# Kernel optimization log

Hardware: AMD Instinct MI355X
Metric: run time of the kernel (lower is better)

Reference implementation:

```python
import jax, jax.numpy as jnp
import numpy as np

B, T, D = 4, 4096, 64

def setup_inputs() -> dict:
    key = jax.random.key(0)
    kq, kk, kv = jax.random.split(key, 3)
    Q = jax.random.normal(kq, (B, T, D), dtype=jnp.float32)
    K = jax.random.normal(kk, (B, T, D), dtype=jnp.float32)
    V = jax.random.normal(kv, (B, T, D), dtype=jnp.float32)
    mask = jnp.zeros((B, T, T), dtype=jnp.float32)
    return {"Q": Q, "K": K, "V": V, "mask": mask}

def reference(Q, K, V, mask):
    dk = Q.shape[-1]
    # NOTE: original scales by 1/dk (not 1/sqrt(dk)) -- reproduce faithfully.
    scores = jnp.einsum('btd,bsd->bts', Q, K) * (1.0 / dk)  # [B,T,T]
    scores = scores + mask
    attn = jax.nn.softmax(scores, axis=-1)
    return jnp.einsum('bts,bsd->btd', attn, V)  # [B,T,D]
```

## Files before the change

kernel.cpp:

```cpp
#include <hip/hip_runtime.h>
#include <stdint.h>

#define BB 4
#define TT 4096
#define DD 64
#define KBLK 64

typedef short short8 __attribute__((ext_vector_type(8)));
typedef float f32x4 __attribute__((ext_vector_type(4)));
typedef uint32_t u32x4 __attribute__((ext_vector_type(4)));

__device__ __forceinline__ uint16_t f2bf(float x) {
  uint32_t u = __float_as_uint(x);
  u += 0x7FFFu + ((u >> 16) & 1u);
  return (uint16_t)(u >> 16);
}
__device__ __forceinline__ float bf2f(uint16_t h) {
  return __uint_as_float(((uint32_t)h) << 16);
}
__device__ __forceinline__ uint32_t pkbf(float a, float b) {
  return (uint32_t)f2bf(a) | ((uint32_t)f2bf(b) << 16);
}

#define MFMA(a, b, c) __builtin_amdgcn_mfma_f32_16x16x32_bf16((a), (b), (c), 0, 0, 0)

__global__ __launch_bounds__(256) void prep_kernel(
    const float* __restrict__ Q, const float* __restrict__ K, const float* __restrict__ V,
    uint16_t* __restrict__ Qh, uint16_t* __restrict__ Ql,
    uint16_t* __restrict__ Kh, uint16_t* __restrict__ Kl,
    uint16_t* __restrict__ Vh, uint16_t* __restrict__ Vl) {
  __shared__ float vt[64][65];
  const int blk = blockIdx.x;
  const int b = blk >> 6;
  const int r0 = (blk & 63) << 6;
  const int t = threadIdx.x;
  const size_t base = ((size_t)b * TT + r0) * DD;
  for (int i = t; i < 64 * 64; i += 256) {
    float q = Q[base + i] * 0.015625f;
    uint16_t h = f2bf(q);
    Qh[base + i] = h;
    Ql[base + i] = f2bf(q - bf2f(h));
    float k = K[base + i];
    h = f2bf(k);
    Kh[base + i] = h;
    Kl[base + i] = f2bf(k - bf2f(h));
    int r = i >> 6, c = i & 63;
    vt[r][c] = V[base + i];
  }
  __syncthreads();
  for (int i = t; i < 64 * 64; i += 256) {
    int d = i >> 6, c = i & 63;
    float v = vt[c][d];
    uint16_t h = f2bf(v);
    size_t o = ((size_t)b * DD + d) * TT + r0 + c;
    Vh[o] = h;
    Vl[o] = f2bf(v - bf2f(h));
  }
}


#define STAGE(KH, KL, VH, VL, S0)                                              \
  do {                                                                         \
    _Pragma("unroll") for (int c = t; c < 512; c += NW * 64) {                 \
      const int cb8 = (c & ~63) * 8;           \
      const int row = c >> 3;                                                  \
      const int ssl = (c & 7) ^ (row & 7);                                     \
      const size_t ksrc = kvb + (size_t)((S0) + row) * DD + ssl * 8;           \
      const size_t vsrc = vtb + (size_t)row * TT + (S0) + ssl * 8;             \
      __builtin_amdgcn_global_load_lds(Kh + ksrc, &KH[cb8], 16, 0, 0);         \
      __builtin_amdgcn_global_load_lds(Kl + ksrc, &KL[cb8], 16, 0, 0);         \
      __builtin_amdgcn_global_load_lds(Vh + vsrc, &VH[cb8], 16, 0, 0);         \
      __builtin_amdgcn_global_load_lds(Vl + vsrc, &VL[cb8], 16, 0, 0);         \
    }                                                                          \
  } while (0)

#define LOADMASK(MK, TILE)                                                     \
  do {                                                                         \
    _Pragma("unroll") for (int q_ = 0; q_ < 4; ++q_)                           \
        MK[q_] = __builtin_nontemporal_load(                                   \
            (const f32x4*)(mprow + (size_t)(TILE) * KBLK + q_ * 16));          \
  } while (0)

#define LOADMASK_Z(MK)                                                         \
  do {                                                                         \
    _Pragma("unroll") for (int q_ = 0; q_ < 4; ++q_)                           \
        MK[q_] = (f32x4){0.f, 0.f, 0.f, 0.f};                                  \
  } while (0)

#define PACK(TT_, HA, HB, LA, LB)                                              \
  {                                                                            \
    const float a0 = s_[TT_][0], a1 = s_[TT_][1];                              \
    const float a2 = s_[TT_][2], a3 = s_[TT_][3];                              \
    const uint16_t h0 = f2bf(a0), h1 = f2bf(a1);                               \
    const uint16_t h2 = f2bf(a2), h3 = f2bf(a3);                               \
    HA = (uint32_t)h0 | ((uint32_t)h1 << 16);                                  \
    HB = (uint32_t)h2 | ((uint32_t)h3 << 16);                                  \
    LA = pkbf(a0 - bf2f(h0), a1 - bf2f(h1));                                   \
    LB = pkbf(a2 - bf2f(h2), a3 - bf2f(h3));                                   \
  }

#define XCHG(W, SA0, SB0, SA1, SB1)                                            \
  {                                                                            \
    const uint32_t A0 = __shfl(SA0, src0), A1 = __shfl(SB0, src0);             \
    const uint32_t B0 = __shfl(SA1, src0), B1 = __shfl(SB1, src0);             \
    const uint32_t A2 = __shfl(SA0, src1), A3 = __shfl(SB0, src1);             \
    const uint32_t B2 = __shfl(SA1, src1), B3 = __shfl(SB1, src1);             \
    W = (u32x4){hi2 ? B0 : A0, hi2 ? B1 : A1, hi2 ? B2 : A2, hi2 ? B3 : A3};   \
  }

#define COMPUTE(KH, KL, VH, VL, MK)                                            \
  do {                                                                         \
    f32x4 s_[4];                                                               \
    _Pragma("unroll") for (int tt = 0; tt < 4; ++tt) {                         \
      f32x4 acc = (f32x4){0.f, 0.f, 0.f, 0.f};                                 \
      const short8 bh0 = *(const short8*)&KH[(tt * 16 + lr) * 64 + sw0 * 8];   \
      const short8 bl0 = *(const short8*)&KL[(tt * 16 + lr) * 64 + sw0 * 8];   \
      acc = MFMA(bh0, qh[0], acc);                                             \
      acc = MFMA(bl0, qh[0], acc);                                             \
      acc = MFMA(bh0, ql[0], acc);                                             \
      const short8 bh1 = *(const short8*)&KH[(tt * 16 + lr) * 64 + sw1 * 8];   \
      const short8 bl1 = *(const short8*)&KL[(tt * 16 + lr) * 64 + sw1 * 8];   \
      acc = MFMA(bh1, qh[1], acc);                                             \
      acc = MFMA(bl1, qh[1], acc);                                             \
      acc = MFMA(bh1, ql[1], acc);                                             \
      s_[tt] = acc + MK[tt];                                                   \
    }                                                                          \
    float cm = fmaxf(fmaxf(fmaxf(s_[0][0], s_[0][1]), fmaxf(s_[0][2], s_[0][3])), \
                     fmaxf(fmaxf(s_[1][0], s_[1][1]), fmaxf(s_[1][2], s_[1][3]))); \
    cm = fmaxf(cm, fmaxf(fmaxf(fmaxf(s_[2][0], s_[2][1]), fmaxf(s_[2][2], s_[2][3])), \
                         fmaxf(fmaxf(s_[3][0], s_[3][1]), fmaxf(s_[3][2], s_[3][3])))); \
    cm = fmaxf(cm, __shfl_xor(cm, 16));                                        \
    cm = fmaxf(cm, __shfl_xor(cm, 32));                                        \
    if (!__all(cm <= mrow + 8.0f)) {                      \
      const float mn = fmaxf(mrow, cm);                                        \
      const float scl = __expf(mrow - mn);                                     \
      mrow = mn;                                                               \
      lrow *= scl;                                                             \
      float sj0 = __shfl(scl, lq * 4 + 0), sj1 = __shfl(scl, lq * 4 + 1);      \
      float sj2 = __shfl(scl, lq * 4 + 2), sj3 = __shfl(scl, lq * 4 + 3);      \
      _Pragma("unroll") for (int dt = 0; dt < 4; ++dt) {                       \
        o[dt][0] *= sj0; o[dt][1] *= sj1; o[dt][2] *= sj2; o[dt][3] *= sj3;    \
      }                                                                        \
    }                                                                          \
    _Pragma("unroll") for (int tt = 0; tt < 4; ++tt)                           \
        _Pragma("unroll") for (int j = 0; j < 4; ++j)                          \
            s_[tt][j] = __expf(s_[tt][j] - mrow);                              \
    float rs = ((s_[0][0] + s_[0][1]) + (s_[0][2] + s_[0][3])) +               \
               ((s_[1][0] + s_[1][1]) + (s_[1][2] + s_[1][3])) +               \
               ((s_[2][0] + s_[2][1]) + (s_[2][2] + s_[2][3])) +               \
               ((s_[3][0] + s_[3][1]) + (s_[3][2] + s_[3][3]));                \
    rs += __shfl_xor(rs, 16);                                                  \
    rs += __shfl_xor(rs, 32);                                                  \
    lrow += rs;                                                                \
    uint32_t H0a, H0b, L0a, L0b, H1a, H1b, L1a, L1b;                           \
    uint32_t H2a, H2b, L2a, L2b, H3a, H3b, L3a, L3b;                           \
    PACK(0, H0a, H0b, L0a, L0b)                                                \
    PACK(1, H1a, H1b, L1a, L1b)                                                \
    PACK(2, H2a, H2b, L2a, L2b)                                                \
    PACK(3, H3a, H3b, L3a, L3b)                                                \
    u32x4 wh0, wl0, wh1, wl1;                                                  \
    XCHG(wh0, H0a, H0b, H1a, H1b)                                              \
    XCHG(wl0, L0a, L0b, L1a, L1b)                                              \
    XCHG(wh1, H2a, H2b, H3a, H3b)                                              \
    XCHG(wl1, L2a, L2b, L3a, L3b)                                              \
    const short8 ph0 = __builtin_bit_cast(short8, wh0);                        \
    const short8 pl0 = __builtin_bit_cast(short8, wl0);                        \
    const short8 ph1 = __builtin_bit_cast(short8, wh1);                        \
    const short8 pl1 = __builtin_bit_cast(short8, wl1);                        \
    _Pragma("unroll") for (int dt = 0; dt < 4; ++dt) {                         \
      const short8 vh = *(const short8*)&VH[(dt * 16 + lr) * 64 + sw0 * 8];    \
      const short8 vl = *(const short8*)&VL[(dt * 16 + lr) * 64 + sw0 * 8];    \
      o[dt] = MFMA(ph0, vh, o[dt]);                                            \
      o[dt] = MFMA(pl0, vh, o[dt]);                                            \
      o[dt] = MFMA(ph0, vl, o[dt]);                                            \
    }                                                                          \
    _Pragma("unroll") for (int dt = 0; dt < 4; ++dt) {                         \
      const short8 vh = *(const short8*)&VH[(dt * 16 + lr) * 64 + sw1 * 8];    \
      const short8 vl = *(const short8*)&VL[(dt * 16 + lr) * 64 + sw1 * 8];    \
      o[dt] = MFMA(ph1, vh, o[dt]);                                            \
      o[dt] = MFMA(pl1, vh, o[dt]);                                            \
      o[dt] = MFMA(ph1, vl, o[dt]);                                            \
    }                                                                          \
  } while (0)

template <int NSEG, int NW>
__global__ __launch_bounds__(NW * 64, 4) void attn_kernel(
    const float* __restrict__ mask, float* __restrict__ out,
    float* __restrict__ Op, float* __restrict__ Mp, float* __restrict__ Lp,
    const uint16_t* __restrict__ Qh, const uint16_t* __restrict__ Ql,
    const uint16_t* __restrict__ Kh, const uint16_t* __restrict__ Kl,
    const uint16_t* __restrict__ Vh, const uint16_t* __restrict__ Vl) {
  constexpr int RPB = NW * 16;
  constexpr int PBH = (TT / RPB) / 2;
  constexpr int SEGLEN = TT / NSEG;
  constexpr int NIT = SEGLEN / KBLK;
  static_assert((NIT & 1) == 0, "NIT must be even for 2x-unrolled dbuf");

  __shared__ uint16_t KhA[4096], KlA[4096], VhA[4096], VlA[4096];
  __shared__ uint16_t KhB[4096], KlB[4096], VhB[4096], VlB[4096];

  const int bid = blockIdx.x;
  const int xcd = bid & 7;
  const int b = xcd >> 1;
  const int u = bid >> 3;
  const int rbl = (u % PBH) * 2 + (xcd & 1);
  const int seg = u / PBH;
  const int q0 = rbl * RPB;
  const int t = threadIdx.x;
  const int w = t >> 6;
  const int l = t & 63;
  const int lr = l & 15;
  const int lq = l >> 4;
  const int qrow = q0 + w * 16;
  const int sb = seg * SEGLEN;

  const int sw0 = lq ^ (lr & 7);
  const int sw1 = sw0 ^ 4;
  const int src0 = lr + (((2 * lq) & 3) << 4);
  const int src1 = lr + (((2 * lq + 1) & 3) << 4);
  const int hi2 = lq >> 1;

  const uint16_t* qhp = Qh + ((size_t)b * TT + qrow + lr) * DD + lq * 8;
  const uint16_t* qlp = Ql + ((size_t)b * TT + qrow + lr) * DD + lq * 8;
  short8 qh[2], ql[2];
  qh[0] = *(const short8*)(qhp);
  qh[1] = *(const short8*)(qhp + 32);
  ql[0] = *(const short8*)(qlp);
  ql[1] = *(const short8*)(qlp + 32);

  f32x4 o[4];
  float mrow = -1e30f, lrow = 0.f;
#pragma unroll
  for (int dt = 0; dt < 4; ++dt) o[dt] = (f32x4){0.f, 0.f, 0.f, 0.f};

  const float* mprow = mask + ((size_t)b * TT + qrow + lr) * TT + sb + lq * 4;
  const size_t kvb = (size_t)b * TT * DD;
  const size_t vtb = (size_t)b * DD * TT;

  f32x4 mk0[4], mk1[4];
  STAGE(KhA, KlA, VhA, VlA, sb);
  LOADMASK(mk0, 0);
  __syncthreads();

  for (int itp = 0; itp < NIT / 2; ++itp) {
    const int it0 = 2 * itp;
    STAGE(KhB, KlB, VhB, VlB, sb + (it0 + 1) * KBLK);
    LOADMASK(mk1, it0 + 1);
    COMPUTE(KhA, KlA, VhA, VlA, mk0);
    __syncthreads();
    if (it0 + 2 < NIT) {
      STAGE(KhA, KlA, VhA, VlA, sb + (it0 + 2) * KBLK);
      LOADMASK(mk0, it0 + 2);
    } else {
      LOADMASK_Z(mk0);
    }
    COMPUTE(KhB, KlB, VhB, VlB, mk1);
    __syncthreads();
  }

  if constexpr (NSEG == 1) {
    const float linv = 1.0f / lrow;
#pragma unroll
    for (int j = 0; j < 4; ++j) {
      const float inv = __shfl(linv, lq * 4 + j);
      const size_t ob = ((size_t)b * TT + qrow + lq * 4 + j) * DD + lr;
#pragma unroll
      for (int dt = 0; dt < 4; ++dt) out[ob + dt * 16] = o[dt][j] * inv;
    }
  } else {
    const int grow = b * TT + qrow;
#pragma unroll
    for (int j = 0; j < 4; ++j) {
      const size_t r = (size_t)seg * (BB * TT) + grow + lq * 4 + j;
#pragma unroll
      for (int dt = 0; dt < 4; ++dt) Op[r * 64 + dt * 16 + lr] = o[dt][j];
    }
    if (lq == 0) {
      const size_t r = (size_t)seg * (BB * TT) + grow + lr;
      Mp[r] = mrow;
      Lp[r] = lrow;
    }
  }
}

__global__ __launch_bounds__(256) void combine_kernel(
    const float* __restrict__ Op, const float* __restrict__ Mp,
    const float* __restrict__ Lp, float* __restrict__ out, int nseg) {
  const int gid = blockIdx.x * 256 + threadIdx.x;
  const int r = gid >> 6, d = gid & 63;
  constexpr int ROWS = BB * TT;
  float m = -3.0e38f;
  for (int s = 0; s < nseg; ++s) m = fmaxf(m, Mp[s * ROWS + r]);
  float num = 0.f, den = 0.f;
  for (int s = 0; s < nseg; ++s) {
    const float e = __expf(Mp[s * ROWS + r] - m);
    den += Lp[s * ROWS + r] * e;
    num += Op[((size_t)s * ROWS + r) * 64 + d] * e;
  }
  out[(size_t)r * 64 + d] = num / den;
}

extern "C" void kernel_launch(void* const* d_in, const int* in_sizes, int n_in,
                              void* d_out, int out_size, void* d_ws, size_t ws_size,
                              hipStream_t stream) {
  const float* Q = (const float*)d_in[0];
  const float* K = (const float*)d_in[1];
  const float* V = (const float*)d_in[2];
  const float* mask = (const float*)d_in[3];
  float* out = (float*)d_out;

  const size_t NE = (size_t)BB * TT * DD;
  const size_t ROWS = (size_t)BB * TT;
  uint16_t* ws = (uint16_t*)d_ws;
  uint16_t* Qh = ws;
  uint16_t* Ql = ws + NE;
  uint16_t* Kh = ws + 2 * NE;
  uint16_t* Kl = ws + 3 * NE;
  uint16_t* Vh = ws + 4 * NE;
  uint16_t* Vl = ws + 5 * NE;

  const size_t bf_bytes = 6 * NE * 2;
  const size_t per_seg = ROWS * 64 * 4 + ROWS * 2 * 4;
  int nseg = (ws_size >= bf_bytes + 4 * per_seg) ? 4
           : (ws_size >= bf_bytes + 2 * per_seg) ? 2 : 1;

  char* pbase = (char*)d_ws + bf_bytes;
  float* Op = (float*)pbase;
  float* Mp = (float*)(pbase + (size_t)nseg * ROWS * 64 * 4);
  float* Lp = Mp + (size_t)nseg * ROWS;

  prep_kernel<<<dim3(256), dim3(256), 0, stream>>>(Q, K, V, Qh, Ql, Kh, Kl, Vh, Vl);

  if (nseg == 4) {
    attn_kernel<4, 8><<<dim3(512), dim3(512), 0, stream>>>(
        mask, out, Op, Mp, Lp, Qh, Ql, Kh, Kl, Vh, Vl);
  } else if (nseg == 2) {
    attn_kernel<2, 8><<<dim3(256), dim3(512), 0, stream>>>(
        mask, out, Op, Mp, Lp, Qh, Ql, Kh, Kl, Vh, Vl);
  } else {
    attn_kernel<1, 4><<<dim3(256), dim3(256), 0, stream>>>(
        mask, out, Op, Mp, Lp, Qh, Ql, Kh, Kl, Vh, Vl);
  }
  if (nseg > 1) {
    combine_kernel<<<dim3((ROWS * 64) / 256), dim3(256), 0, stream>>>(Op, Mp, Lp, out, nseg);
  }
}
```

Measured before the change: 404.6 us.

## Process two 16-row query tiles per wave to reuse K/V LDS fragments

Each wave now handles 32 query rows as two independent 16-row tiles, so every K and V fragment read from LDS feeds MFMAs for both tiles. Workgroups shrink from 8 to 4 waves with the same total rows per block, and the launch-bounds occupancy hint drops from 4 to 2. Mask loads for the next tile are moved inside the softmax step to overlap with compute. The aim is to halve LDS read traffic per MFMA and add independent MFMA chains, at the cost of more registers and lower occupancy.

```diff
diff --git a/kernel.cpp b/kernel.cpp
--- a/kernel.cpp
+++ b/kernel.cpp
@@ -74,23 +74,17 @@
     }                                                                          \
   } while (0)
 
-#define LOADMASK(MK, TILE)                                                     \
+#define LOADMASK(MK, MPR, TILE)                                                \
   do {                                                                         \
     _Pragma("unroll") for (int q_ = 0; q_ < 4; ++q_)                           \
         MK[q_] = __builtin_nontemporal_load(                                   \
-            (const f32x4*)(mprow + (size_t)(TILE) * KBLK + q_ * 16));          \
+            (const f32x4*)((MPR) + (size_t)(TILE) * KBLK + q_ * 16));          \
   } while (0)
 
-#define LOADMASK_Z(MK)                                                         \
-  do {                                                                         \
-    _Pragma("unroll") for (int q_ = 0; q_ < 4; ++q_)                           \
-        MK[q_] = (f32x4){0.f, 0.f, 0.f, 0.f};                                  \
-  } while (0)
-
-#define PACK(TT_, HA, HB, LA, LB)                                              \
+#define PACK(S, TT_, HA, HB, LA, LB)                                           \
   {                                                                            \
-    const float a0 = s_[TT_][0], a1 = s_[TT_][1];                              \
-    const float a2 = s_[TT_][2], a3 = s_[TT_][3];                              \
+    const float a0 = S[TT_][0], a1 = S[TT_][1];                                \
+    const float a2 = S[TT_][2], a3 = S[TT_][3];                                \
     const uint16_t h0 = f2bf(a0), h1 = f2bf(a1);                               \
     const uint16_t h2 = f2bf(a2), h3 = f2bf(a3);                               \
     HA = (uint32_t)h0 | ((uint32_t)h1 << 16);                                  \
@@ -108,89 +102,104 @@
     W = (u32x4){hi2 ? B0 : A0, hi2 ? B1 : A1, hi2 ? B2 : A2, hi2 ? B3 : A3};   \
   }
 
-#define COMPUTE(KH, KL, VH, VL, MK)                                            \
+#define SMPACK(S, MK, MPR, MROW, LROW, O, PH, PL, TNEXT)                       \
   do {                                                                         \
-    f32x4 s_[4];                                                               \
-    _Pragma("unroll") for (int tt = 0; tt < 4; ++tt) {                         \
-      f32x4 acc = (f32x4){0.f, 0.f, 0.f, 0.f};                                 \
-      const short8 bh0 = *(const short8*)&KH[(tt * 16 + lr) * 64 + sw0 * 8];   \
-      const short8 bl0 = *(const short8*)&KL[(tt * 16 + lr) * 64 + sw0 * 8];   \
-      acc = MFMA(bh0, qh[0], acc);                                             \
-      acc = MFMA(bl0, qh[0], acc);                                             \
-      acc = MFMA(bh0, ql[0], acc);                                             \
-      const short8 bh1 = *(const short8*)&KH[(tt * 16 + lr) * 64 + sw1 * 8];   \
-      const short8 bl1 = *(const short8*)&KL[(tt * 16 + lr) * 64 + sw1 * 8];   \
-      acc = MFMA(bh1, qh[1], acc);                                             \
-      acc = MFMA(bl1, qh[1], acc);                                             \
-      acc = MFMA(bh1, ql[1], acc);                                             \
-      s_[tt] = acc + MK[tt];                                                   \
-    }                                                                          \
-    float cm = fmaxf(fmaxf(fmaxf(s_[0][0], s_[0][1]), fmaxf(s_[0][2], s_[0][3])), \
-                     fmaxf(fmaxf(s_[1][0], s_[1][1]), fmaxf(s_[1][2], s_[1][3]))); \
-    cm = fmaxf(cm, fmaxf(fmaxf(fmaxf(s_[2][0], s_[2][1]), fmaxf(s_[2][2], s_[2][3])), \
-                         fmaxf(fmaxf(s_[3][0], s_[3][1]), fmaxf(s_[3][2], s_[3][3])))); \
+    float cm = fmaxf(fmaxf(fmaxf(S[0][0], S[0][1]), fmaxf(S[0][2], S[0][3])),  \
+                     fmaxf(fmaxf(S[1][0], S[1][1]), fmaxf(S[1][2], S[1][3]))); \
+    cm = fmaxf(cm, fmaxf(fmaxf(fmaxf(S[2][0], S[2][1]), fmaxf(S[2][2], S[2][3])), \
+                         fmaxf(fmaxf(S[3][0], S[3][1]), fmaxf(S[3][2], S[3][3])))); \
     cm = fmaxf(cm, __shfl_xor(cm, 16));                                        \
     cm = fmaxf(cm, __shfl_xor(cm, 32));                                        \
-    if (!__all(cm <= mrow + 8.0f)) {                      \
-      const float mn = fmaxf(mrow, cm);                                        \
-      const float scl = __expf(mrow - mn);                                     \
-      mrow = mn;                                                               \
-      lrow *= scl;                                                             \
+    if (!__all(cm <= MROW + 8.0f)) {                      \
+      const float mn = fmaxf(MROW, cm);                                        \
+      const float scl = __expf(MROW - mn);                                     \
+      MROW = mn;                                                               \
+      LROW *= scl;                                                             \
       float sj0 = __shfl(scl, lq * 4 + 0), sj1 = __shfl(scl, lq * 4 + 1);      \
       float sj2 = __shfl(scl, lq * 4 + 2), sj3 = __shfl(scl, lq * 4 + 3);      \
       _Pragma("unroll") for (int dt = 0; dt < 4; ++dt) {                       \
-        o[dt][0] *= sj0; o[dt][1] *= sj1; o[dt][2] *= sj2; o[dt][3] *= sj3;    \
+        O[dt][0] *= sj0; O[dt][1] *= sj1; O[dt][2] *= sj2; O[dt][3] *= sj3;    \
       }                                                                        \
     }                                                                          \
     _Pragma("unroll") for (int tt = 0; tt < 4; ++tt)                           \
         _Pragma("unroll") for (int j = 0; j < 4; ++j)                          \
-            s_[tt][j] = __expf(s_[tt][j] - mrow);                              \
-    float rs = ((s_[0][0] + s_[0][1]) + (s_[0][2] + s_[0][3])) +               \
-               ((s_[1][0] + s_[1][1]) + (s_[1][2] + s_[1][3])) +               \
-               ((s_[2][0] + s_[2][1]) + (s_[2][2] + s_[2][3])) +               \
-               ((s_[3][0] + s_[3][1]) + (s_[3][2] + s_[3][3]));                \
+            S[tt][j] = __expf(S[tt][j] - MROW);                                \
+    float rs = ((S[0][0] + S[0][1]) + (S[0][2] + S[0][3])) +                   \
+               ((S[1][0] + S[1][1]) + (S[1][2] + S[1][3])) +                   \
+               ((S[2][0] + S[2][1]) + (S[2][2] + S[2][3])) +                   \
+               ((S[3][0] + S[3][1]) + (S[3][2] + S[3][3]));                    \
     rs += __shfl_xor(rs, 16);                                                  \
     rs += __shfl_xor(rs, 32);                                                  \
-    lrow += rs;                                                                \
+    LROW += rs;                                                                \
+    LOADMASK(MK, MPR, TNEXT);     \
     uint32_t H0a, H0b, L0a, L0b, H1a, H1b, L1a, L1b;                           \
     uint32_t H2a, H2b, L2a, L2b, H3a, H3b, L3a, L3b;                           \
-    PACK(0, H0a, H0b, L0a, L0b)                                                \
-    PACK(1, H1a, H1b, L1a, L1b)                                                \
-    PACK(2, H2a, H2b, L2a, L2b)                                                \
-    PACK(3, H3a, H3b, L3a, L3b)                                                \
+    PACK(S, 0, H0a, H0b, L0a, L0b)                                             \
+    PACK(S, 1, H1a, H1b, L1a, L1b)                                             \
+    PACK(S, 2, H2a, H2b, L2a, L2b)                                             \
+    PACK(S, 3, H3a, H3b, L3a, L3b)                                             \
     u32x4 wh0, wl0, wh1, wl1;                                                  \
     XCHG(wh0, H0a, H0b, H1a, H1b)                                              \
     XCHG(wl0, L0a, L0b, L1a, L1b)                                              \
     XCHG(wh1, H2a, H2b, H3a, H3b)                                              \
     XCHG(wl1, L2a, L2b, L3a, L3b)                                              \
-    const short8 ph0 = __builtin_bit_cast(short8, wh0);                        \
-    const short8 pl0 = __builtin_bit_cast(short8, wl0);                        \
-    const short8 ph1 = __builtin_bit_cast(short8, wh1);                        \
-    const short8 pl1 = __builtin_bit_cast(short8, wl1);                        \
-    _Pragma("unroll") for (int dt = 0; dt < 4; ++dt) {                         \
-      const short8 vh = *(const short8*)&VH[(dt * 16 + lr) * 64 + sw0 * 8];    \
-      const short8 vl = *(const short8*)&VL[(dt * 16 + lr) * 64 + sw0 * 8];    \
-      o[dt] = MFMA(ph0, vh, o[dt]);                                            \
-      o[dt] = MFMA(pl0, vh, o[dt]);                                            \
-      o[dt] = MFMA(ph0, vl, o[dt]);                                            \
+    PH[0] = __builtin_bit_cast(short8, wh0);                                   \
+    PL[0] = __builtin_bit_cast(short8, wl0);                                   \
+    PH[1] = __builtin_bit_cast(short8, wh1);                                   \
+    PL[1] = __builtin_bit_cast(short8, wl1);                                   \
+  } while (0)
+
+#define COMPUTE(KH, KL, VH, VL, TNEXT)                                         \
+  do {                                                                         \
+    f32x4 s0_[4], s1_[4];                                                      \
+    _Pragma("unroll") for (int tt = 0; tt < 4; ++tt) {                         \
+      f32x4 a0 = (f32x4){0.f, 0.f, 0.f, 0.f};                                  \
+      f32x4 a1 = (f32x4){0.f, 0.f, 0.f, 0.f};                                  \
+      const short8 bh0 = *(const short8*)&KH[(tt * 16 + lr) * 64 + sw0 * 8];   \
+      const short8 bl0 = *(const short8*)&KL[(tt * 16 + lr) * 64 + sw0 * 8];   \
+      a0 = MFMA(bh0, qh0[0], a0);                                              \
+      a0 = MFMA(bl0, qh0[0], a0);                                              \
+      a0 = MFMA(bh0, ql0[0], a0);                                              \
+      a1 = MFMA(bh0, qh1[0], a1);                                              \
+      a1 = MFMA(bl0, qh1[0], a1);                                              \
+      a1 = MFMA(bh0, ql1[0], a1);                                              \
+      const short8 bh1 = *(const short8*)&KH[(tt * 16 + lr) * 64 + sw1 * 8];   \
+      const short8 bl1 = *(const short8*)&KL[(tt * 16 + lr) * 64 + sw1 * 8];   \
+      a0 = MFMA(bh1, qh0[1], a0);                                              \
+      a0 = MFMA(bl1, qh0[1], a0);                                              \
+      a0 = MFMA(bh1, ql0[1], a0);                                              \
+      a1 = MFMA(bh1, qh1[1], a1);                                              \
+      a1 = MFMA(bl1, qh1[1], a1);                                              \
+      a1 = MFMA(bh1, ql1[1], a1);                                              \
+      s0_[tt] = a0 + mk0[tt];                                                  \
+      s1_[tt] = a1 + mk1[tt];                                                  \
     }                                                                          \
-    _Pragma("unroll") for (int dt = 0; dt < 4; ++dt) {                         \
-      const short8 vh = *(const short8*)&VH[(dt * 16 + lr) * 64 + sw1 * 8];    \
-      const short8 vl = *(const short8*)&VL[(dt * 16 + lr) * 64 + sw1 * 8];    \
-      o[dt] = MFMA(ph1, vh, o[dt]);                                            \
-      o[dt] = MFMA(pl1, vh, o[dt]);                                            \
-      o[dt] = MFMA(ph1, vl, o[dt]);                                            \
+    SMPACK(s0_, mk0, mpr0, m0, l0, o0, ph0, pl0, TNEXT);                       \
+    SMPACK(s1_, mk1, mpr1, m1, l1, o1, ph1, pl1, TNEXT);                       \
+    _Pragma("unroll") for (int c = 0; c < 2; ++c) {                            \
+      const int sw = c ? sw1 : sw0;                                            \
+      _Pragma("unroll") for (int dt = 0; dt < 4; ++dt) {                       \
+        const short8 vh = *(const short8*)&VH[(dt * 16 + lr) * 64 + sw * 8];   \
+        const short8 vl = *(const short8*)&VL[(dt * 16 + lr) * 64 + sw * 8];   \
+        o0[dt] = MFMA(ph0[c], vh, o0[dt]);                                     \
+        o0[dt] = MFMA(pl0[c], vh, o0[dt]);                                     \
+        o0[dt] = MFMA(ph0[c], vl, o0[dt]);                                     \
+        o1[dt] = MFMA(ph1[c], vh, o1[dt]);                                     \
+        o1[dt] = MFMA(pl1[c], vh, o1[dt]);                                     \
+        o1[dt] = MFMA(ph1[c], vl, o1[dt]);                                     \
+      }                                                                        \
     }                                                                          \
   } while (0)
 
 template <int NSEG, int NW>
-__global__ __launch_bounds__(NW * 64, 4) void attn_kernel(
+__global__ __launch_bounds__(NW * 64, 2) void attn_kernel(
     const float* __restrict__ mask, float* __restrict__ out,
     float* __restrict__ Op, float* __restrict__ Mp, float* __restrict__ Lp,
     const uint16_t* __restrict__ Qh, const uint16_t* __restrict__ Ql,
     const uint16_t* __restrict__ Kh, const uint16_t* __restrict__ Kl,
     const uint16_t* __restrict__ Vh, const uint16_t* __restrict__ Vl) {
-  constexpr int RPB = NW * 16;
+  constexpr int RPW = 32;
+  constexpr int RPB = NW * RPW;
   constexpr int PBH = (TT / RPB) / 2;
   constexpr int SEGLEN = TT / NSEG;
   constexpr int NIT = SEGLEN / KBLK;
@@ -211,7 +220,7 @@
   const int l = t & 63;
   const int lr = l & 15;
   const int lq = l >> 4;
-  const int qrow = q0 + w * 16;
+  const int qbase = q0 + w * RPW;
   const int sb = seg * SEGLEN;
 
   const int sw0 = lq ^ (lr & 7);
@@ -220,65 +229,85 @@
   const int src1 = lr + (((2 * lq + 1) & 3) << 4);
   const int hi2 = lq >> 1;
 
-  const uint16_t* qhp = Qh + ((size_t)b * TT + qrow + lr) * DD + lq * 8;
-  const uint16_t* qlp = Ql + ((size_t)b * TT + qrow + lr) * DD + lq * 8;
-  short8 qh[2], ql[2];
-  qh[0] = *(const short8*)(qhp);
-  qh[1] = *(const short8*)(qhp + 32);
-  ql[0] = *(const short8*)(qlp);
-  ql[1] = *(const short8*)(qlp + 32);
-
-  f32x4 o[4];
-  float mrow = -1e30f, lrow = 0.f;
-#pragma unroll
-  for (int dt = 0; dt < 4; ++dt) o[dt] = (f32x4){0.f, 0.f, 0.f, 0.f};
-
-  const float* mprow = mask + ((size_t)b * TT + qrow + lr) * TT + sb + lq * 4;
+  const size_t qoff0 = ((size_t)b * TT + qbase + lr) * DD + lq * 8;
+  const size_t qoff1 = qoff0 + 16 * DD;
+  short8 qh0[2], ql0[2], qh1[2], ql1[2];
+  qh0[0] = *(const short8*)(Qh + qoff0);
+  qh0[1] = *(const short8*)(Qh + qoff0 + 32);
+  ql0[0] = *(const short8*)(Ql + qoff0);
+  ql0[1] = *(const short8*)(Ql + qoff0 + 32);
+  qh1[0] = *(const short8*)(Qh + qoff1);
+  qh1[1] = *(const short8*)(Qh + qoff1 + 32);
+  ql1[0] = *(const short8*)(Ql + qoff1);
+  ql1[1] = *(const short8*)(Ql + qoff1 + 32);
+
+  f32x4 o0[4], o1[4];
+  float m0 = -1e30f, l0 = 0.f, m1 = -1e30f, l1 = 0.f;
+#pragma unroll
+  for (int dt = 0; dt < 4; ++dt) {
+    o0[dt] = (f32x4){0.f, 0.f, 0.f, 0.f};
+    o1[dt] = (f32x4){0.f, 0.f, 0.f, 0.f};
+  }
+
+  const float* mpr0 = mask + ((size_t)b * TT + qbase + lr) * TT + sb + lq * 4;
+  const float* mpr1 = mpr0 + (size_t)16 * TT;
   const size_t kvb = (size_t)b * TT * DD;
   const size_t vtb = (size_t)b * DD * TT;
 
+  short8 ph0[2], pl0[2], ph1[2], pl1[2];
   f32x4 mk0[4], mk1[4];
+
   STAGE(KhA, KlA, VhA, VlA, sb);
-  LOADMASK(mk0, 0);
+  LOADMASK(mk0, mpr0, 0);
+  LOADMASK(mk1, mpr1, 0);
   __syncthreads();
 
   for (int itp = 0; itp < NIT / 2; ++itp) {
     const int it0 = 2 * itp;
     STAGE(KhB, KlB, VhB, VlB, sb + (it0 + 1) * KBLK);
-    LOADMASK(mk1, it0 + 1);
-    COMPUTE(KhA, KlA, VhA, VlA, mk0);
+    {
+      const int tn = (it0 + 1 < NIT) ? it0 + 1 : 0;
+      COMPUTE(KhA, KlA, VhA, VlA, tn);
+    }
     __syncthreads();
-    if (it0 + 2 < NIT) {
-      STAGE(KhA, KlA, VhA, VlA, sb + (it0 + 2) * KBLK);
-      LOADMASK(mk0, it0 + 2);
-    } else {
-      LOADMASK_Z(mk0);
-    }
-    COMPUTE(KhB, KlB, VhB, VlB, mk1);
+    if (it0 + 2 < NIT) STAGE(KhA, KlA, VhA, VlA, sb + (it0 + 2) * KBLK);
+    {
+      const int tn = (it0 + 2 < NIT) ? it0 + 2 : 0;
+      COMPUTE(KhB, KlB, VhB, VlB, tn);
+    }
     __syncthreads();
   }
 
   if constexpr (NSEG == 1) {
-    const float linv = 1.0f / lrow;
+    const float li0 = 1.0f / l0, li1 = 1.0f / l1;
 #pragma unroll
     for (int j = 0; j < 4; ++j) {
-      const float inv = __shfl(linv, lq * 4 + j);
-      const size_t ob = ((size_t)b * TT + qrow + lq * 4 + j) * DD + lr;
-#pragma unroll
-      for (int dt = 0; dt < 4; ++dt) out[ob + dt * 16] = o[dt][j] * inv;
+      const float i0 = __shfl(li0, lq * 4 + j);
+      const float i1 = __shfl(li1, lq * 4 + j);
+      const size_t ob0 = ((size_t)b * TT + qbase + lq * 4 + j) * DD + lr;
+#pragma unroll
+      for (int dt = 0; dt < 4; ++dt) {
+        out[ob0 + dt * 16] = o0[dt][j] * i0;
+        out[ob0 + (size_t)16 * DD + dt * 16] = o1[dt][j] * i1;
+      }
     }
   } else {
-    const int grow = b * TT + qrow;
+    const int grow = b * TT + qbase;
 #pragma unroll
     for (int j = 0; j < 4; ++j) {
-      const size_t r = (size_t)seg * (BB * TT) + grow + lq * 4 + j;
-#pragma unroll
-      for (int dt = 0; dt < 4; ++dt) Op[r * 64 + dt * 16 + lr] = o[dt][j];
+      const size_t r0 = (size_t)seg * (BB * TT) + grow + lq * 4 + j;
+#pragma unroll
+      for (int dt = 0; dt < 4; ++dt) {
+        Op[r0 * 64 + dt * 16 + lr] = o0[dt][j];
+        Op[(r0 + 16) * 64 + dt * 16 + lr] = o1[dt][j];
+      }
     }
     if (lq == 0) {
       const size_t r = (size_t)seg * (BB * TT) + grow + lr;
-      Mp[r] = mrow;
-      Lp[r] = lrow;
+      Mp[r] = m0;
+      Lp[r] = l0;
+      Mp[r + 16] = m1;
+      Lp[r + 16] = l1;
     }
   }
 }
@@ -332,13 +361,13 @@
   prep_kernel<<<dim3(256), dim3(256), 0, stream>>>(Q, K, V, Qh, Ql, Kh, Kl, Vh, Vl);
 
   if (nseg == 4) {
-    attn_kernel<4, 8><<<dim3(512), dim3(512), 0, stream>>>(
+    attn_kernel<4, 4><<<dim3(512), dim3(256), 0, stream>>>(
         mask, out, Op, Mp, Lp, Qh, Ql, Kh, Kl, Vh, Vl);
   } else if (nseg == 2) {
-    attn_kernel<2, 8><<<dim3(256), dim3(512), 0, stream>>>(
+    attn_kernel<2, 4><<<dim3(256), dim3(256), 0, stream>>>(
         mask, out, Op, Mp, Lp, Qh, Ql, Kh, Kl, Vh, Vl);
   } else {
-    attn_kernel<1, 4><<<dim3(256), dim3(256), 0, stream>>>(
+    attn_kernel<1, 4><<<dim3(128), dim3(256), 0, stream>>>(
         mask, out, Op, Mp, Lp, Qh, Ql, Kh, Kl, Vh, Vl);
   }
   if (nseg > 1) {
```

After: 409.1 us. About the same (+1.1%).
